# Optimization experiments

Hardware: AMD Instinct MI355X
Metric: run time of the kernel (lower is better)

Reference implementation:

```python
import jax, jax.numpy as jnp
import numpy as np

SCALE = 2
GROUPS = 4


def setup_inputs() -> dict:
    key = jax.random.key(0)
    k1, k2 = jax.random.split(key, 2)
    B, C, H, W = 8, 256, 96, 96
    out_ch = 2 * GROUPS * SCALE ** 2  # 32
    x = jax.random.normal(k1, (B, C, H, W), dtype=jnp.float32)
    # offset conv: normal_init(std=0.001), bias=0
    w = jax.random.normal(k2, (out_ch, C), dtype=jnp.float32) * 0.001
    b = jnp.zeros((out_ch,), dtype=jnp.float32)
    return {"x": x, "w": w, "b": b}


def _grid_sample_bilinear_border(x, grid):
    """x: [N,C,H,W]; grid: [N,Ho,Wo,2] with (x,y) in [-1,1]; align_corners=False,
    padding_mode='border' (coords clamped to [0, size-1] before interpolation)."""
    N, C, H, W = x.shape
    Ho, Wo = grid.shape[1], grid.shape[2]
    gx = (grid[..., 0] + 1.0) * (W * 0.5) - 0.5
    gy = (grid[..., 1] + 1.0) * (H * 0.5) - 0.5
    gx = jnp.clip(gx, 0.0, W - 1.0)
    gy = jnp.clip(gy, 0.0, H - 1.0)
    x0 = jnp.floor(gx)
    y0 = jnp.floor(gy)
    wx = (gx - x0).reshape(N, 1, Ho * Wo)
    wy = (gy - y0).reshape(N, 1, Ho * Wo)
    x0i = x0.astype(jnp.int32)
    y0i = y0.astype(jnp.int32)
    x1i = jnp.minimum(x0i + 1, W - 1)
    y1i = jnp.minimum(y0i + 1, H - 1)
    xf = x.reshape(N, C, H * W)

    def gather(yi, xi):
        idx = (yi * W + xi).reshape(N, 1, Ho * Wo)
        return jnp.take_along_axis(xf, idx, axis=2)  # [N,C,Ho*Wo]

    v00 = gather(y0i, x0i)
    v01 = gather(y0i, x1i)
    v10 = gather(y1i, x0i)
    v11 = gather(y1i, x1i)
    out = (v00 * (1.0 - wx) * (1.0 - wy) + v01 * wx * (1.0 - wy)
           + v10 * (1.0 - wx) * wy + v11 * wx * wy)
    return out.reshape(N, C, Ho, Wo)


def reference(x, w, b):
    B, C, H, W = x.shape
    r, g = SCALE, GROUPS
    # 1x1 conv producing per-pixel offsets
    off = jnp.einsum('bchw,oc->bohw', x, w) + b[None, :, None, None]  # [B,32,H,W]
    Co = off.shape[1] // (r * r)  # 2*groups = 8
    # pixel_shuffle(r): out[b,c,h*r+i,w*r+j] = in[b, c*r*r + i*r + j, h, w]
    off = off.reshape(B, Co, r, r, H, W).transpose(0, 1, 4, 2, 5, 3)
    off = off.reshape(B, Co, H * r, W * r)
    off = jnp.tanh(off)
    Hs, Ws = H * r, W * r
    xr = x.reshape(B * g, C // g, H, W)
    off_field = off.reshape(B * g, 2, Hs, Ws).transpose(0, 2, 3, 1)  # [B*g,Hs,Ws,2]
    ry = jnp.linspace(-1.0 + 1.0 / Hs, 1.0 - 1.0 / Hs, Hs, dtype=jnp.float32)
    rx = jnp.linspace(-1.0 + 1.0 / Ws, 1.0 - 1.0 / Ws, Ws, dtype=jnp.float32)
    gy, gx = jnp.meshgrid(ry, rx, indexing='ij')
    base = jnp.stack([gx, gy], axis=-1)[None]  # [1,Hs,Ws,2]
    grid = base + off_field * 0.125
    out = _grid_sample_bilinear_border(xr, grid)
    return out.reshape(B, C, Hs, Ws)
```

## Files before the change

### kernel.cpp

```cpp
#include <hip/hip_runtime.h>

#define Cc  256
#define Hh  96
#define Ww  96
#define HW  (Hh*Ww)
#define OC  32
#define HS  192
#define WSS 192
#define PLANE (HS*WSS)

__global__ __launch_bounds__(256) void conv_offset_kernel(
    const float* __restrict__ x, const float* __restrict__ w,
    const float* __restrict__ bias, float* __restrict__ grid_buf)
{
    __shared__ float lds[Cc * OC];
    const int tid   = threadIdx.x;
    const int pix   = tid & 63;
    const int slice = tid >> 6;

    for (int l = tid; l < Cc * OC; l += 256) {
        int cc = l >> 5, oo = l & 31;
        lds[l] = w[oo * Cc + cc];
    }
    __syncthreads();

    const int p  = blockIdx.x * 64 + pix;
    const int b  = p / HW;
    const int hw = p - b * HW;
    const float* xp = x + (size_t)b * Cc * HW + (size_t)(slice * 64) * HW + hw;

    float acc[OC];
    #pragma unroll
    for (int o = 0; o < OC; ++o) acc[o] = 0.0f;

    const float* wrow = &lds[slice * 64 * OC];
    #pragma unroll 4
    for (int c = 0; c < 64; ++c) {
        float xv = xp[(size_t)c * HW];
        const float4* wr4 = (const float4*)&wrow[c * OC];
        #pragma unroll
        for (int o4 = 0; o4 < 8; ++o4) {
            float4 wv = wr4[o4];
            acc[4*o4+0] = fmaf(wv.x, xv, acc[4*o4+0]);
            acc[4*o4+1] = fmaf(wv.y, xv, acc[4*o4+1]);
            acc[4*o4+2] = fmaf(wv.z, xv, acc[4*o4+2]);
            acc[4*o4+3] = fmaf(wv.w, xv, acc[4*o4+3]);
        }
    }

    __syncthreads();
    #pragma unroll
    for (int o = 0; o < OC; ++o) lds[(o * 4 + slice) * 64 + pix] = acc[o];
    __syncthreads();

    const int h  = hw / Ww;
    const int ww = hw - h * Ww;
    const int obase = slice * 8;
    #pragma unroll
    for (int oo = 0; oo < 8; ++oo) {
        const int o = obase + oo;
        float s = lds[(o * 4 + 0) * 64 + pix]
                + lds[(o * 4 + 1) * 64 + pix]
                + lds[(o * 4 + 2) * 64 + pix]
                + lds[(o * 4 + 3) * 64 + pix] + bias[o];
        const int co  = o >> 2;
        const int rem = o & 3;
        const int i   = rem >> 1;
        const int j   = rem & 1;
        const int gr  = co >> 1;
        const int k   = co & 1;
        const int hs  = 2 * h + i;
        const int ws  = 2 * ww + j;
        float t = tanhf(s);
        float coord = (k == 0) ? (0.5f * (float)ws - 0.25f + 6.0f * t)
                               : (0.5f * (float)hs - 0.25f + 6.0f * t);
        coord = fminf(fmaxf(coord, 0.0f), 95.0f);
        const int bg = b * 4 + gr;
        grid_buf[(((size_t)bg * HS + hs) * WSS + ws) * 2 + k] = coord;
    }
}

__global__ __launch_bounds__(256) void sample_kernel(
    const float* __restrict__ x, const float* __restrict__ grid_buf,
    float* __restrict__ out)
{
    __shared__ float pl[9344];
    const int bc  = blockIdx.x;
    const int b   = bc >> 8;
    const int c   = bc & 255;
    const int bg  = b * 4 + (c >> 6);
    const int tid = threadIdx.x;

    const float4* xp4 = (const float4*)(x + (size_t)bc * HW);
    float4* pl4 = (float4*)pl;
    #pragma unroll
    for (int i = 0; i < 9; ++i) pl4[tid + 256 * i] = xp4[tid + 256 * i];
    if (tid < 128) pl[9216 + tid] = 0.0f;
    __syncthreads();

    const float* gbase = grid_buf + (size_t)bg * PLANE * 2;
    float* obase = out + (size_t)bc * PLANE;

    for (int r = 0; r < 36; ++r) {
        const int idx = r * 1024 + tid * 4;
        const float4* gp = (const float4*)(gbase + (size_t)idx * 2);
        float4 g01 = gp[0];
        float4 g23 = gp[1];
        float gx[4] = {g01.x, g01.z, g23.x, g23.z};
        float gy[4] = {g01.y, g01.w, g23.y, g23.w};
        float res[4];
        #pragma unroll
        for (int q = 0; q < 4; ++q) {
            float fx = gx[q], fy = gy[q];
            float x0f = floorf(fx), y0f = floorf(fy);
            float wx = fx - x0f, wy = fy - y0f;
            int base = (int)fmaf(y0f, 96.0f, x0f);
            float a0 = pl[base],      a1 = pl[base + 1];
            float b0 = pl[base + 96], b1 = pl[base + 97];
            float top = a0 + (a1 - a0) * wx;
            float bot = b0 + (b1 - b0) * wx;
            res[q] = top + (bot - top) * wy;
        }
        *(float4*)(obase + idx) = make_float4(res[0], res[1], res[2], res[3]);
    }
}

extern "C" void kernel_launch(void* const* d_in, const int* in_sizes, int n_in,
                              void* d_out, int out_size, void* d_ws, size_t ws_size,
                              hipStream_t stream) {
    const float* x    = (const float*)d_in[0];
    const float* w    = (const float*)d_in[1];
    const float* bias = (const float*)d_in[2];
    float* out        = (float*)d_out;
    float* grid_buf   = (float*)d_ws;

    conv_offset_kernel<<<1152, 256, 0, stream>>>(x, w, bias, grid_buf);
    sample_kernel<<<2048, 256, 0, stream>>>(x, grid_buf, out);
}
```

Measured before the change: 463.1 us.

## Pre-transpose conv weights and sample two channels per block with interleaved LDS

Adds a small kernel that transposes the 1x1 conv weights once into workspace, so the conv kernel reads weights straight from global memory with a wave-uniform slice instead of staging all 32 KB into LDS per block. The sample kernel now processes two channels per block with 512 threads, storing the two planes interleaved as float2 in LDS. Each grid coordinate read and its bilinear index math is then shared by both channels, halving grid_buf traffic. The cost is an extra launch, 73 KB of LDS per sample block (lower occupancy), and scalar rather than float4 output stores.

Result: faster. 388.8 us (-16.0%).

```diff
diff --git a/kernel.cpp b/kernel.cpp
--- a/kernel.cpp
+++ b/kernel.cpp
@@ -8,39 +8,42 @@
 #define HS  192
 #define WSS 192
 #define PLANE (HS*WSS)
+#define WT_FLOATS (Cc*OC)
+
+__global__ __launch_bounds__(256) void transpose_w_kernel(
+    const float* __restrict__ w, float* __restrict__ wt)
+{
+    const int l = blockIdx.x * 256 + threadIdx.x;
+    const int o = l >> 8, c = l & 255;
+    wt[c * OC + o] = w[l];
+}
 
 __global__ __launch_bounds__(256) void conv_offset_kernel(
-    const float* __restrict__ x, const float* __restrict__ w,
+    const float* __restrict__ x, const float* __restrict__ wt,
     const float* __restrict__ bias, float* __restrict__ grid_buf)
 {
     __shared__ float lds[Cc * OC];
     const int tid   = threadIdx.x;
     const int pix   = tid & 63;
-    const int slice = tid >> 6;
-
-    for (int l = tid; l < Cc * OC; l += 256) {
-        int cc = l >> 5, oo = l & 31;
-        lds[l] = w[oo * Cc + cc];
-    }
-    __syncthreads();
+    const int slice = __builtin_amdgcn_readfirstlane(threadIdx.x >> 6);
 
     const int p  = blockIdx.x * 64 + pix;
     const int b  = p / HW;
     const int hw = p - b * HW;
     const float* xp = x + (size_t)b * Cc * HW + (size_t)(slice * 64) * HW + hw;
+    const float* wp = wt + slice * (64 * OC);
 
     float acc[OC];
     #pragma unroll
     for (int o = 0; o < OC; ++o) acc[o] = 0.0f;
 
-    const float* wrow = &lds[slice * 64 * OC];
     #pragma unroll 4
     for (int c = 0; c < 64; ++c) {
         float xv = xp[(size_t)c * HW];
-        const float4* wr4 = (const float4*)&wrow[c * OC];
+        const float4* w4 = (const float4*)&wp[c * OC];
         #pragma unroll
         for (int o4 = 0; o4 < 8; ++o4) {
-            float4 wv = wr4[o4];
+            float4 wv = w4[o4];
             acc[4*o4+0] = fmaf(wv.x, xv, acc[4*o4+0]);
             acc[4*o4+1] = fmaf(wv.y, xv, acc[4*o4+1]);
             acc[4*o4+2] = fmaf(wv.z, xv, acc[4*o4+2]);
@@ -48,7 +51,6 @@
         }
     }
 
-    __syncthreads();
     #pragma unroll
     for (int o = 0; o < OC; ++o) lds[(o * 4 + slice) * 64 + pix] = acc[o];
     __syncthreads();
@@ -80,48 +82,52 @@
     }
 }
 
-__global__ __launch_bounds__(256) void sample_kernel(
+__global__ __launch_bounds__(512) void sample_kernel(
     const float* __restrict__ x, const float* __restrict__ grid_buf,
     float* __restrict__ out)
 {
-    __shared__ float pl[9344];
-    const int bc  = blockIdx.x;
-    const int b   = bc >> 8;
-    const int c   = bc & 255;
-    const int bg  = b * 4 + (c >> 6);
+    __shared__ __align__(16) float2 pl[9344];
+    const int bp  = blockIdx.x;
+    const int b   = bp >> 7;
+    const int c2  = (bp & 127) << 1;
+    const int bg  = b * 4 + (c2 >> 6);
     const int tid = threadIdx.x;
 
-    const float4* xp4 = (const float4*)(x + (size_t)bc * HW);
+    const float4* xp0 = (const float4*)(x + (size_t)(b * 256 + c2) * HW);
+    const float4* xp1 = (const float4*)(x + (size_t)(b * 256 + c2 + 1) * HW);
     float4* pl4 = (float4*)pl;
     #pragma unroll
-    for (int i = 0; i < 9; ++i) pl4[tid + 256 * i] = xp4[tid + 256 * i];
-    if (tid < 128) pl[9216 + tid] = 0.0f;
+    for (int i = 0; i < 5; ++i) {
+        int t = tid + 512 * i;
+        if (i < 4 || t < 2304) {
+            float4 a = xp0[t];
+            float4 bb = xp1[t];
+            pl4[2 * t]     = make_float4(a.x, bb.x, a.y, bb.y);
+            pl4[2 * t + 1] = make_float4(a.z, bb.z, a.w, bb.w);
+        }
+    }
+    if (tid < 128) pl[9216 + tid] = make_float2(0.0f, 0.0f);
     __syncthreads();
 
     const float* gbase = grid_buf + (size_t)bg * PLANE * 2;
-    float* obase = out + (size_t)bc * PLANE;
+    float* ob0 = out + (size_t)(b * 256 + c2) * PLANE;
+    float* ob1 = ob0 + PLANE;
 
-    for (int r = 0; r < 36; ++r) {
-        const int idx = r * 1024 + tid * 4;
-        const float4* gp = (const float4*)(gbase + (size_t)idx * 2);
-        float4 g01 = gp[0];
-        float4 g23 = gp[1];
-        float gx[4] = {g01.x, g01.z, g23.x, g23.z};
-        float gy[4] = {g01.y, g01.w, g23.y, g23.w};
-        float res[4];
-        #pragma unroll
-        for (int q = 0; q < 4; ++q) {
-            float fx = gx[q], fy = gy[q];
-            float x0f = floorf(fx), y0f = floorf(fy);
-            float wx = fx - x0f, wy = fy - y0f;
-            int base = (int)fmaf(y0f, 96.0f, x0f);
-            float a0 = pl[base],      a1 = pl[base + 1];
-            float b0 = pl[base + 96], b1 = pl[base + 97];
-            float top = a0 + (a1 - a0) * wx;
-            float bot = b0 + (b1 - b0) * wx;
-            res[q] = top + (bot - top) * wy;
-        }
-        *(float4*)(obase + idx) = make_float4(res[0], res[1], res[2], res[3]);
+    #pragma unroll 2
+    for (int r = 0; r < 72; ++r) {
+        const int idx = r * 512 + tid;
+        float2 g = *(const float2*)(gbase + (size_t)idx * 2);
+        float x0f = floorf(g.x), y0f = floorf(g.y);
+        float wx = g.x - x0f, wy = g.y - y0f;
+        int base = (int)fmaf(y0f, 96.0f, x0f);
+        float2 a0 = pl[base],      a1 = pl[base + 1];
+        float2 b0 = pl[base + 96], b1 = pl[base + 97];
+        float top0 = a0.x + (a1.x - a0.x) * wx;
+        float bot0 = b0.x + (b1.x - b0.x) * wx;
+        ob0[idx] = top0 + (bot0 - top0) * wy;
+        float top1 = a0.y + (a1.y - a0.y) * wx;
+        float bot1 = b0.y + (b1.y - b0.y) * wx;
+        ob1[idx] = top1 + (bot1 - top1) * wy;
     }
 }
 
@@ -132,8 +138,10 @@
     const float* w    = (const float*)d_in[1];
     const float* bias = (const float*)d_in[2];
     float* out        = (float*)d_out;
-    float* grid_buf   = (float*)d_ws;
+    float* wt         = (float*)d_ws;
+    float* grid_buf   = wt + WT_FLOATS;
 
-    conv_offset_kernel<<<1152, 256, 0, stream>>>(x, w, bias, grid_buf);
-    sample_kernel<<<2048, 256, 0, stream>>>(x, grid_buf, out);
+    transpose_w_kernel<<<32, 256, 0, stream>>>(w, wt);
+    conv_offset_kernel<<<1152, 256, 0, stream>>>(x, wt, bias, grid_buf);
+    sample_kernel<<<1024, 512, 0, stream>>>(x, grid_buf, out);
 }
```
